# Performance work log

Measured on AMD Instinct MI355X. Metric: run time of the kernel, lower is better.

## Reference

```python
import jax, jax.numpy as jnp
import numpy as np

NUM_CODEBOOK = 2048
EMBED_DIM = 64
BETA = 0.25


def _l2norm(x, eps=1e-12):
    # F.normalize(x, dim=1): x / max(||x||, eps)
    n = jnp.sqrt(jnp.sum(x * x, axis=1, keepdims=True))
    return x / jnp.maximum(n, eps)


def setup_inputs() -> dict:
    key = jax.random.key(0)
    k1, k2 = jax.random.split(key)
    z = jax.random.normal(k1, (16, EMBED_DIM, 64, 64), dtype=jnp.float32)
    # xavier_normal_ init for (K, d) embedding weight
    std = float(np.sqrt(2.0 / (NUM_CODEBOOK + EMBED_DIM)))
    codebook = jax.random.normal(k2, (NUM_CODEBOOK, EMBED_DIM), dtype=jnp.float32) * std
    return {"z": z, "codebook": codebook}


def reference(z, codebook):
    b, d, h, w = z.shape
    z_bhwd = jnp.transpose(z, (0, 2, 3, 1))          # (b,h,w,d)
    z_flat = z_bhwd.reshape(-1, d)                   # (n,d)

    # normalize == 'l2'
    z_norm = _l2norm(z_flat)
    codebook_norm = _l2norm(codebook)                # (K,d)

    # squared euclidean distance: ||z||^2 + ||c||^2 - 2 z c^T  -> (n,K)
    distance = (jnp.sum(z_norm * z_norm, axis=1, keepdims=True)
                + jnp.sum(codebook_norm * codebook_norm, axis=1)
                - 2.0 * jnp.matmul(z_norm, codebook_norm.T))

    vq_indices = jnp.argmin(distance, axis=1)        # (n,)
    distance_prob = jax.nn.softmax(-distance, axis=1)

    z_q = codebook_norm[vq_indices]                  # (n,d) embedding gather

    codebook_loss = jnp.mean((z_q - jax.lax.stop_gradient(z_norm)) ** 2)
    commitment_loss = jnp.mean((z_norm - jax.lax.stop_gradient(z_q)) ** 2)
    loss = codebook_loss + BETA * commitment_loss

    # straight-through estimator
    z_q_st = z_norm + jax.lax.stop_gradient(z_q - z_norm)
    q = jnp.transpose(z_q_st.reshape(b, h, w, d), (0, 3, 1, 2))  # (b,d,h,w)
    return q, loss, codebook_loss, commitment_loss, distance_prob
```

## Files before the change

### kernel.cpp

```cpp
#include <hip/hip_runtime.h>

typedef _Float16 f16x8 __attribute__((ext_vector_type(8)));
typedef float f32x4 __attribute__((ext_vector_type(4)));

#define NN 65536
#define KK 2048
#define DD 64

__device__ __forceinline__ unsigned int fkey(float f) {
  unsigned int u = __float_as_uint(f);
  return (u & 0x80000000u) ? ~u : (u | 0x80000000u);
}

__global__ void k_norm_cb(const float* __restrict__ cb, float* __restrict__ cbT32,
                          float* __restrict__ cn2,
                          unsigned short* __restrict__ Bhi,
                          unsigned short* __restrict__ Blo) {
  int gid = blockIdx.x * blockDim.x + threadIdx.x;
  int c = gid >> 6;
  int k = gid & 63;
  float v = cb[c * DD + k];
  float ss = v * v;
  #pragma unroll
  for (int o = 32; o; o >>= 1) ss += __shfl_xor(ss, o);
  float inv = 1.0f / fmaxf(sqrtf(ss), 1e-12f);
  float cn = v * inv;
  cbT32[k * KK + c] = cn;
  float s2 = cn * cn;
  #pragma unroll
  for (int o = 32; o; o >>= 1) s2 += __shfl_xor(s2, o);
  if (k == 0) cn2[c] = s2;
  float sh = cn * 256.0f;
  _Float16 hh = (_Float16)sh;
  float resid = sh - (float)hh;
  _Float16 hl = (_Float16)(resid * 4096.0f);
  int s = k >> 5, g2 = (k >> 3) & 3, i = k & 7;
  int idx = s * 65536 + c * 32 + g2 * 8 + i;
  Bhi[idx] = *(unsigned short*)&hh;
  Blo[idx] = *(unsigned short*)&hl;
}

__global__ void k_norm_z(const float* __restrict__ z,
                         unsigned short* __restrict__ Ahi,
                         unsigned short* __restrict__ Alo) {
  __shared__ float np_[8][32];
  __shared__ float invS[32];
  int t = threadIdx.x;
  int r32 = t & 31, q = t >> 5;
  int n0 = blockIdx.x * 32;
  int w0 = n0 & 63, hh = (n0 >> 6) & 63, bb = n0 >> 12;
  const float* src = z + (size_t)bb * 262144 + (size_t)q * 8 * 4096 + hh * 64 + w0 + r32;
  float v[8];
  float ss = 0.f;
  #pragma unroll
  for (int i = 0; i < 8; ++i) {
    float x = src[(size_t)i * 4096];
    v[i] = x;
    ss = fmaf(x, x, ss);
  }
  np_[q][r32] = ss;
  __syncthreads();
  if (t < 32) {
    float s = 0.f;
    #pragma unroll
    for (int qq = 0; qq < 8; ++qq) s += np_[qq][t];
    invS[t] = 1.0f / fmaxf(sqrtf(s), 1e-12f);
  }
  __syncthreads();
  float inv = invS[r32] * 256.0f;
  union { _Float16 h[8]; uint4 u; } hi, lo;
  #pragma unroll
  for (int i = 0; i < 8; ++i) {
    float sh = v[i] * inv;
    _Float16 a = (_Float16)sh;
    hi.h[i] = a;
    lo.h[i] = (_Float16)((sh - (float)a) * 4096.0f);
  }
  int rt = (n0 + r32) >> 4;
  int r = r32 & 15;
  int s = q >> 2, g2 = q & 3;
  size_t idx = (size_t)(rt * 2 + s) * 64 + g2 * 16 + r;
  ((uint4*)Ahi)[idx] = hi.u;
  ((uint4*)Alo)[idx] = lo.u;
}

__global__ __launch_bounds__(1024) void k_main(
    const f16x8* __restrict__ Ahi, const f16x8* __restrict__ Alo,
    const f16x8* __restrict__ Bhi, const f16x8* __restrict__ Blo,
    const float* __restrict__ cn2g, const float* __restrict__ cbT32,
    float* __restrict__ qout, float* __restrict__ prob,
    float* __restrict__ partials) {
  __shared__ unsigned long long keyS[16];
  __shared__ float rowpart[16][16];
  __shared__ float rowInv[16];
  __shared__ float wsum[16];

  int t = threadIdx.x;
  int lane = t & 63, wv = t >> 6;
  int l15 = lane & 15, g = lane >> 4;
  int rt = blockIdx.x;
  int n0 = rt * 16;
  int wc0 = wv * 128;

  if (t < 16) keyS[t] = ~0ull;

  f16x8 a_hi[2], a_lo[2];
  {
    size_t base = (size_t)rt * 128 + (size_t)g * 16 + l15;
    a_hi[0] = Ahi[base];      a_hi[1] = Ahi[base + 64];
    a_lo[0] = Alo[base];      a_lo[1] = Alo[base + 64];
  }

  f32x4 acc1[8], acc2[8];
  #pragma unroll
  for (int i = 0; i < 8; ++i) {
    acc1[i] = (f32x4){0.f, 0.f, 0.f, 0.f};
    acc2[i] = (f32x4){0.f, 0.f, 0.f, 0.f};
  }

  int b0 = (wc0 + l15) * 4 + g;
  f16x8 bhA = Bhi[b0], blA = Blo[b0];
  f16x8 bhB, blB;
  #pragma unroll
  for (int p = 0; p < 16; ++p) {
    int t8 = p >> 1, s = p & 1;
    if (p < 15) {
      int pn = p + 1;
      int idxn = (pn & 1) * 8192 + (pn >> 1) * 64 + b0;
      if (p & 1) { bhA = Bhi[idxn]; blA = Blo[idxn]; }
      else       { bhB = Bhi[idxn]; blB = Blo[idxn]; }
    }
    f16x8 bh = (p & 1) ? bhB : bhA;
    f16x8 bl = (p & 1) ? blB : blA;
    acc2[t8] = __builtin_amdgcn_mfma_f32_16x16x32_f16(a_lo[s], bh, acc2[t8], 0, 0, 0);
    acc1[t8] = __builtin_amdgcn_mfma_f32_16x16x32_f16(a_hi[s], bh, acc1[t8], 0, 0, 0);
    acc2[t8] = __builtin_amdgcn_mfma_f32_16x16x32_f16(a_hi[s], bl, acc2[t8], 0, 0, 0);
  }

  unsigned long long kmin[4] = {~0ull, ~0ull, ~0ull, ~0ull};
  float esum[4] = {0.f, 0.f, 0.f, 0.f};
  #pragma unroll
  for (int t8 = 0; t8 < 8; ++t8) {
    int col = wc0 + t8 * 16 + l15;
    float c2 = cn2g[col];
    #pragma unroll
    for (int r = 0; r < 4; ++r) {
      float dot = fmaf(acc2[t8][r], 3.7252903e-09f, acc1[t8][r] * 1.52587890625e-05f);
      float d = fmaf(-2.0f, dot, c2);
      unsigned long long kk = ((unsigned long long)fkey(d) << 32) | (unsigned)col;
      if (kk < kmin[r]) kmin[r] = kk;
      float e = __expf(-d);
      acc1[t8][r] = e;
      esum[r] += e;
    }
  }
  #pragma unroll
  for (int o = 1; o <= 8; o <<= 1) {
    #pragma unroll
    for (int r = 0; r < 4; ++r) {
      esum[r] += __shfl_xor(esum[r], o);
      unsigned long long ok = __shfl_xor(kmin[r], o);
      if (ok < kmin[r]) kmin[r] = ok;
    }
  }
  __syncthreads();
  if (l15 == 0) {
    #pragma unroll
    for (int r = 0; r < 4; ++r) {
      rowpart[g * 4 + r][wv] = esum[r];
      atomicMin(&keyS[g * 4 + r], kmin[r]);
    }
  }
  __syncthreads();
  if (t < 16) {
    float s = 0.f;
    #pragma unroll
    for (int w = 0; w < 16; ++w) s += rowpart[t][w];
    rowInv[t] = 1.0f / s;
  }
  __syncthreads();

  {
    float4 inv4 = *(const float4*)&rowInv[g * 4];
    float* pp = prob + (size_t)(n0 + g * 4) * KK + wc0 + l15;
    #pragma unroll
    for (int t8 = 0; t8 < 8; ++t8) {
      float* p0 = pp + t8 * 16;
      p0[0]          = acc1[t8][0] * inv4.x;
      p0[KK]         = acc1[t8][1] * inv4.y;
      p0[2 * KK]     = acc1[t8][2] * inv4.z;
      p0[3 * KK]     = acc1[t8][3] * inv4.w;
    }
  }

  {
    int r = t & 15, k = t >> 4;
    int cw = (int)(keyS[r] & 0xffffffffull);
    float qv = cbT32[k * KK + cw];
    int w0 = n0 & 63, hh2 = (n0 >> 6) & 63, bb = n0 >> 12;
    qout[((size_t)((bb << 6) | k) * 64 + hh2) * 64 + w0 + r] = qv;
    size_t aidx = ((size_t)(rt * 2 + (k >> 5)) * 64 + ((k >> 3) & 3) * 16 + r) * 8 + (k & 7);
    float ah = (float)((const _Float16*)Ahi)[aidx];
    float al = (float)((const _Float16*)Alo)[aidx];
    float zn = fmaf(al, 2.44140625e-04f, ah) * 3.90625e-03f;
    float df = qv - zn;
    float ssd = df * df;
    #pragma unroll
    for (int o = 32; o; o >>= 1) ssd += __shfl_xor(ssd, o);
    if (lane == 0) wsum[wv] = ssd;
  }
  __syncthreads();
  if (t == 0) {
    float s = 0.f;
    #pragma unroll
    for (int w = 0; w < 16; ++w) s += wsum[w];
    partials[rt] = s;
  }
}

__global__ void k_final(const float* __restrict__ partials, float* __restrict__ out) {
  __shared__ float wsh[4];
  int t = threadIdx.x;
  float s = 0.f;
  for (int i = 0; i < 16; ++i) s += partials[t * 16 + i];
  #pragma unroll
  for (int o = 32; o; o >>= 1) s += __shfl_xor(s, o);
  if ((t & 63) == 0) wsh[t >> 6] = s;
  __syncthreads();
  if (t == 0) {
    float tot = (wsh[0] + wsh[1]) + (wsh[2] + wsh[3]);
    float cbl = tot * (1.0f / 4194304.0f);
    out[4194304] = 1.25f * cbl;
    out[4194305] = cbl;
    out[4194306] = cbl;
  }
}

extern "C" void kernel_launch(void* const* d_in, const int* in_sizes, int n_in,
                              void* d_out, int out_size, void* d_ws, size_t ws_size,
                              hipStream_t stream) {
  const float* z = (const float*)d_in[0];
  const float* cb = (const float*)d_in[1];
  float* out = (float*)d_out;
  char* ws = (char*)d_ws;

  float* cbT32 = (float*)(ws);
  float* cn2 = (float*)(ws + 524288);
  unsigned short* Bhi = (unsigned short*)(ws + 532480);
  unsigned short* Blo = (unsigned short*)(ws + 794624);
  float* partials = (float*)(ws + 1056768);
  unsigned short* Ahi = (unsigned short*)(ws + 1073152);
  unsigned short* Alo = (unsigned short*)(ws + 9461760);

  k_norm_cb<<<512, 256, 0, stream>>>(cb, cbT32, cn2, Bhi, Blo);
  k_norm_z<<<2048, 256, 0, stream>>>(z, Ahi, Alo);
  k_main<<<4096, 1024, 0, stream>>>((const f16x8*)Ahi, (const f16x8*)Alo,
                                    (const f16x8*)Bhi, (const f16x8*)Blo,
                                    cn2, cbT32, out, out + 4194307, partials);
  k_final<<<1, 256, 0, stream>>>(partials, out);
}
```

Measured before the change: 328.2 us.

## Swap MFMA operand order so each lane owns one row for vectorized prob stores

Swaps the A and B operands of the MFMA so the accumulator is transposed: each lane now holds four consecutive codebook columns for a single row. The per-row min and sum reductions drop from 4 values over 4 shuffle steps to 1 value over 2 steps, the cn2 load becomes a float4, and the prob output is written with 16-byte vector stores instead of scalar strided stores. The output write is the dominant memory cost, so wider stores should improve coalescing, at the cost of a changed lane-to-column mapping that has to stay consistent with the argmin tie-break order.

```diff
diff --git a/kernel.cpp b/kernel.cpp
--- a/kernel.cpp
+++ b/kernel.cpp
@@ -104,11 +104,11 @@
 
   if (t < 16) keyS[t] = ~0ull;
 
-  f16x8 a_hi[2], a_lo[2];
+  f16x8 z_hi[2], z_lo[2];
   {
     size_t base = (size_t)rt * 128 + (size_t)g * 16 + l15;
-    a_hi[0] = Ahi[base];      a_hi[1] = Ahi[base + 64];
-    a_lo[0] = Alo[base];      a_lo[1] = Alo[base + 64];
+    z_hi[0] = Ahi[base];      z_hi[1] = Ahi[base + 64];
+    z_lo[0] = Alo[base];      z_lo[1] = Alo[base + 64];
   }
 
   f32x4 acc1[8], acc2[8];
@@ -132,44 +132,40 @@
     }
     f16x8 bh = (p & 1) ? bhB : bhA;
     f16x8 bl = (p & 1) ? blB : blA;
-    acc2[t8] = __builtin_amdgcn_mfma_f32_16x16x32_f16(a_lo[s], bh, acc2[t8], 0, 0, 0);
-    acc1[t8] = __builtin_amdgcn_mfma_f32_16x16x32_f16(a_hi[s], bh, acc1[t8], 0, 0, 0);
-    acc2[t8] = __builtin_amdgcn_mfma_f32_16x16x32_f16(a_hi[s], bl, acc2[t8], 0, 0, 0);
-  }
-
-  unsigned long long kmin[4] = {~0ull, ~0ull, ~0ull, ~0ull};
-  float esum[4] = {0.f, 0.f, 0.f, 0.f};
+    acc2[t8] = __builtin_amdgcn_mfma_f32_16x16x32_f16(bh, z_lo[s], acc2[t8], 0, 0, 0);
+    acc1[t8] = __builtin_amdgcn_mfma_f32_16x16x32_f16(bh, z_hi[s], acc1[t8], 0, 0, 0);
+    acc2[t8] = __builtin_amdgcn_mfma_f32_16x16x32_f16(bl, z_hi[s], acc2[t8], 0, 0, 0);
+  }
+
+  unsigned long long kmin = ~0ull;
+  float esum = 0.f;
+  int cb0 = wc0 + g * 4;
   #pragma unroll
   for (int t8 = 0; t8 < 8; ++t8) {
-    int col = wc0 + t8 * 16 + l15;
-    float c2 = cn2g[col];
+    int c0 = cb0 + t8 * 16;
+    float4 c4 = *(const float4*)(cn2g + c0);
+    float cn[4] = {c4.x, c4.y, c4.z, c4.w};
     #pragma unroll
     for (int r = 0; r < 4; ++r) {
       float dot = fmaf(acc2[t8][r], 3.7252903e-09f, acc1[t8][r] * 1.52587890625e-05f);
-      float d = fmaf(-2.0f, dot, c2);
-      unsigned long long kk = ((unsigned long long)fkey(d) << 32) | (unsigned)col;
-      if (kk < kmin[r]) kmin[r] = kk;
+      float d = fmaf(-2.0f, dot, cn[r]);
+      unsigned long long kk = ((unsigned long long)fkey(d) << 32) | (unsigned)(c0 + r);
+      if (kk < kmin) kmin = kk;
       float e = __expf(-d);
       acc1[t8][r] = e;
-      esum[r] += e;
+      esum += e;
     }
   }
   #pragma unroll
-  for (int o = 1; o <= 8; o <<= 1) {
-    #pragma unroll
-    for (int r = 0; r < 4; ++r) {
-      esum[r] += __shfl_xor(esum[r], o);
-      unsigned long long ok = __shfl_xor(kmin[r], o);
-      if (ok < kmin[r]) kmin[r] = ok;
-    }
-  }
-  __syncthreads();
-  if (l15 == 0) {
-    #pragma unroll
-    for (int r = 0; r < 4; ++r) {
-      rowpart[g * 4 + r][wv] = esum[r];
-      atomicMin(&keyS[g * 4 + r], kmin[r]);
-    }
+  for (int o = 16; o <= 32; o <<= 1) {
+    esum += __shfl_xor(esum, o);
+    unsigned long long ok = __shfl_xor(kmin, o);
+    if (ok < kmin) kmin = ok;
+  }
+  __syncthreads();
+  if (lane < 16) {
+    rowpart[l15][wv] = esum;
+    atomicMin(&keyS[l15], kmin);
   }
   __syncthreads();
   if (t < 16) {
@@ -181,15 +177,12 @@
   __syncthreads();
 
   {
-    float4 inv4 = *(const float4*)&rowInv[g * 4];
-    float* pp = prob + (size_t)(n0 + g * 4) * KK + wc0 + l15;
+    float inv = rowInv[l15];
+    float* pp = prob + (size_t)(n0 + l15) * KK + cb0;
     #pragma unroll
     for (int t8 = 0; t8 < 8; ++t8) {
-      float* p0 = pp + t8 * 16;
-      p0[0]          = acc1[t8][0] * inv4.x;
-      p0[KK]         = acc1[t8][1] * inv4.y;
-      p0[2 * KK]     = acc1[t8][2] * inv4.z;
-      p0[3 * KK]     = acc1[t8][3] * inv4.w;
+      f32x4 o4 = acc1[t8] * inv;
+      *(f32x4*)(pp + t8 * 16) = o4;
     }
   }
 
```

New measurement: 317.4 us. 1.03x faster.
